# Performance work log

Measured on AMD Instinct MI355X. Metric: run time of the kernel, lower is better.

## Reference

```python
import jax, jax.numpy as jnp
import numpy as np

# ---- static config (matches init_kwargs and NSA hyperparams in source) ----
DIM = 512; HEADS = 8; DH = DIM // HEADS; DEPTH = 2
HH = 28; WW = 28; SEQ = HH * WW            # 784
WIN = 28 * 7                                # sliding window = 196
CBS = 28 * 14; CST = 28 * 7                 # compress block 392, stride 196
SBS = 28 * 14; NSEL = 1                     # selection block 392, top-1
NC = (SEQ - CBS) // CST + 1                 # 3 compressed blocks
NS = SEQ // SBS                             # 2 selection blocks
EPS = 1e-5
BATCH = 8


def _overlap_matrix():
    # fraction of each compressed block overlapping each selection block
    O = np.zeros((NC, NS), np.float32)
    for i in range(NC):
        a, b = i * CST, i * CST + CBS
        for j in range(NS):
            c, d = j * SBS, (j + 1) * SBS
            O[i, j] = max(0, min(b, d) - max(a, c)) / CBS
    return jnp.asarray(O)

OVERLAP = _overlap_matrix()  # [NC, NS]


def setup_inputs() -> dict:
    key = jax.random.key(0)
    ks = jax.random.split(key, 12)
    p = lambda i, shape, s=0.02: (jax.random.normal(ks[i], shape, jnp.float32) * s)
    return {
        "x": jax.random.normal(ks[0], (BATCH, DIM, HH, WW), jnp.float32),
        "pos_emb": jax.random.normal(ks[1], (SEQ,), jnp.float32),
        "attn_norm_g": jnp.ones((DEPTH, DIM), jnp.float32),
        "Wq": p(2, (DEPTH, DIM, HEADS * DH)),
        "Wk": p(3, (DEPTH, DIM, HEADS * DH)),
        "Wv": p(4, (DEPTH, DIM, HEADS * DH)),
        "Wo": p(5, (DEPTH, HEADS * DH, DIM)),
        "Wg": p(6, (DEPTH, DIM, HEADS * 3)),
        "ff_norm_g": jnp.ones((DEPTH, DIM), jnp.float32),
        "ff_norm_b": jnp.zeros((DEPTH, DIM), jnp.float32),
        "ff_w1": p(7, (DEPTH, 4 * DIM, DIM)),
        "ff_b1": jnp.zeros((DEPTH, 4 * DIM), jnp.float32),
        "ff_w2": p(8, (DEPTH, DIM, 4 * DIM)),
        "ff_b2": jnp.zeros((DEPTH, DIM), jnp.float32),
    }


def _sparse_attn(x, g, wq, wk, wv, wo, wg):
    # x: [b, n, d]  -- NSA: sliding window + compressed + top-k block selection
    b, n, d = x.shape
    xr = x * jax.lax.rsqrt(jnp.mean(x * x, -1, keepdims=True) + EPS) * g  # RMSNorm
    q = (xr @ wq).reshape(b, n, HEADS, DH)
    k = (xr @ wk).reshape(b, n, HEADS, DH)
    v = (xr @ wv).reshape(b, n, HEADS, DH)
    scale = DH ** -0.5

    # ---- compressed branch: mean-pool overlapping blocks ----
    ck = jnp.stack([k[:, i * CST:i * CST + CBS].mean(1) for i in range(NC)], 1)  # [b,NC,h,dh]
    cv = jnp.stack([v[:, i * CST:i * CST + CBS].mean(1) for i in range(NC)], 1)
    sc = jnp.einsum('bihd,bjhd->bhij', q, ck) * scale          # [b,h,n,NC]
    pc = jax.nn.softmax(sc, -1)
    out_c = jnp.einsum('bhij,bjhd->bihd', pc, cv)              # [b,n,h,dh]

    # ---- selection branch: importance -> top-k selection blocks -> fine attn ----
    imp = jnp.einsum('bhij,jk->bhik', pc, OVERLAP)             # [b,h,n,NS]
    _, sel = jax.lax.top_k(imp, NSEL)                          # [b,h,n,NSEL]
    selmask = jax.nn.one_hot(sel, NS, dtype=jnp.float32).sum(-2) > 0  # [b,h,n,NS]
    blk = jnp.arange(n) // SBS                                 # token -> selection block
    tokmask = selmask[..., blk]                                # [b,h,n,n]
    sf = jnp.einsum('bihd,bjhd->bhij', q, k) * scale           # full fine scores (shared)
    neg = jnp.finfo(sf.dtype).min
    ps = jax.nn.softmax(jnp.where(tokmask, sf, neg), -1)
    out_s = jnp.einsum('bhij,bjhd->bihd', ps, v)

    # ---- sliding window branch ----
    idx = jnp.arange(n)
    winmask = jnp.abs(idx[:, None] - idx[None, :]) < WIN       # [n,n]
    pw = jax.nn.softmax(jnp.where(winmask, sf, neg), -1)
    out_w = jnp.einsum('bhij,bjhd->bihd', pw, v)

    # ---- per-head learned gates over the 3 branches ----
    gates = jax.nn.sigmoid(xr @ wg).reshape(b, n, HEADS, 3)
    o = (gates[..., 0:1] * out_c + gates[..., 1:2] * out_s + gates[..., 2:3] * out_w)
    return o.reshape(b, n, HEADS * DH) @ wo


def _ff(x, g, bb, w1, b1, w2, b2):
    # x: [b,c,h,w]; LayerNorm over channel dim, then 1x1 conv -> GELU -> 1x1 conv
    mean = x.mean(1, keepdims=True)
    var = jnp.var(x, 1, keepdims=True)
    xn = (x - mean) / jnp.sqrt(var + EPS) * g[None, :, None, None] + bb[None, :, None, None]
    h1 = jax.nn.gelu(jnp.einsum('bchw,oc->bohw', xn, w1) + b1[None, :, None, None], approximate=False)
    return jnp.einsum('bchw,oc->bohw', h1, w2) + b2[None, :, None, None]


def reference(x, pos_emb, attn_norm_g, Wq, Wk, Wv, Wo, Wg,
              ff_norm_g, ff_norm_b, ff_w1, ff_b1, ff_w2, ff_b2):
    b, c, h, w = x.shape
    x = x + pos_emb[:h * w].reshape(1, 1, h, w)
    for l in range(DEPTH):
        s = x.reshape(b, c, h * w).transpose(0, 2, 1)          # b (h w) c
        s = _sparse_attn(s, attn_norm_g[l], Wq[l], Wk[l], Wv[l], Wo[l], Wg[l]) + s
        x = s.transpose(0, 2, 1).reshape(b, c, h, w)
        x = _ff(x, ff_norm_g[l], ff_norm_b[l], ff_w1[l], ff_b1[l], ff_w2[l], ff_b2[l]) + x
    return x
```

## Files before the change

kernel.cpp:

```cpp
#include <hip/hip_runtime.h>
#include <hip/hip_bf16.h>
#include <math.h>

#define B_      8
#define DIMC    512
#define SEQ_    784
#define HEADS_  8
#define DH_     64
#define NTOK    (B_*SEQ_)
#define QLD     1560
#define WIN_    196
#define CBS_    392
#define CST_    196
#define NC_     3
#define EPSF    1e-5f
#define FF_     2048
#define TQ_     28
#define MT_     98

typedef __hip_bfloat16 bf16_t;
typedef __attribute__((ext_vector_type(8))) short bf16x8;
typedef __attribute__((ext_vector_type(4))) float floatx4;
typedef __attribute__((ext_vector_type(4))) unsigned int uintx4;
typedef __attribute__((ext_vector_type(2))) unsigned int uintx2;

__device__ __forceinline__ float wsum(float x){
#pragma unroll
  for (int o = 32; o; o >>= 1) x += __shfl_xor(x, o, 64);
  return x;
}
__device__ __forceinline__ float geluf(float x){
  return 0.5f * x * (1.0f + erff(x * 0.70710678118654752f));
}
__device__ __forceinline__ float sigmoidf_(float x){
  return 1.0f / (1.0f + __expf(-x));
}

__global__ __launch_bounds__(256) void k_init(const float* __restrict__ xin,
                                              const float* __restrict__ pos,
                                              float* __restrict__ X){
  int idx = blockIdx.x * 256 + threadIdx.x;
  int c = idx & 511;
  int t = idx >> 9;
  int p = t % SEQ_;
  int b = t / SEQ_;
  float v = xin[((long)(b * DIMC + c)) * SEQ_ + p];
  X[idx] = v + pos[p];
}

__global__ __launch_bounds__(256) void k_final(const float* __restrict__ X,
                                               float* __restrict__ out){
  int idx = blockIdx.x * 256 + threadIdx.x;
  int p = idx % SEQ_;
  int t = idx / SEQ_;
  int c = t & 511;
  int b = t >> 9;
  out[idx] = X[((long)(b * SEQ_ + p)) * DIMC + c];
}

__global__ __launch_bounds__(256) void k_wconv1(const float* __restrict__ Wq,
                                                const float* __restrict__ Wk,
                                                const float* __restrict__ Wv,
                                                const float* __restrict__ Wg,
                                                bf16_t* __restrict__ Wb){
  int idx = blockIdx.x * 256 + threadIdx.x;
  int k = idx & 511;
  int t = idx >> 9;
  int n = t % QLD;
  int l = t / QLD;
  float v;
  if (n < 1536){
    int which = n >> 9;
    int nn = n & 511;
    const float* W = (which == 0) ? Wq : ((which == 1) ? Wk : Wv);
    v = W[((long)(l * 512 + k)) * 512 + nn];
  } else {
    v = Wg[((long)(l * 512 + k)) * 24 + (n - 1536)];
  }
  Wb[idx] = __float2bfloat16(v);
}

__global__ __launch_bounds__(256) void k_wconv2(const float* __restrict__ Wo,
                                                bf16_t* __restrict__ Wb){
  int idx = blockIdx.x * 256 + threadIdx.x;
  int k = idx & 511;
  int t = idx >> 9;
  int n = t & 511;
  int l = t >> 9;
  Wb[idx] = __float2bfloat16(Wo[((long)(l * 512 + k)) * 512 + n]);
}

__global__ __launch_bounds__(256) void k_cast(const float* __restrict__ src,
                                              bf16_t* __restrict__ dst){
  int idx = blockIdx.x * 256 + threadIdx.x;
  dst[idx] = __float2bfloat16(src[idx]);
}

__global__ __launch_bounds__(256) void k_zero(uintx4* __restrict__ p){
  p[blockIdx.x * 256 + threadIdx.x] = (uintx4){0u, 0u, 0u, 0u};
}

__global__ __launch_bounds__(256) void k_rms(const float* __restrict__ X,
                                             const float* __restrict__ g,
                                             bf16_t* __restrict__ XR){
  int tok = blockIdx.x;
  int tid = threadIdx.x;
  const float* xr = X + (long)tok * DIMC;
  float v0 = xr[tid], v1 = xr[tid + 256];
  float ss = v0 * v0 + v1 * v1;
  ss = wsum(ss);
  __shared__ float red[4];
  if ((tid & 63) == 0) red[tid >> 6] = ss;
  __syncthreads();
  float tot = red[0] + red[1] + red[2] + red[3];
  float r = rsqrtf(tot * (1.0f / DIMC) + EPSF);
  XR[(long)tok * DIMC + tid]       = __float2bfloat16(v0 * r * g[tid]);
  XR[(long)tok * DIMC + tid + 256] = __float2bfloat16(v1 * r * g[tid + 256]);
}

__global__ __launch_bounds__(256) void k_ln(const float* __restrict__ X,
                                            const float* __restrict__ g,
                                            const float* __restrict__ bb,
                                            bf16_t* __restrict__ XN){
  int tok = blockIdx.x;
  int tid = threadIdx.x;
  const float* xr = X + (long)tok * DIMC;
  float v0 = xr[tid], v1 = xr[tid + 256];
  float s = v0 + v1;
  float q = v0 * v0 + v1 * v1;
  s = wsum(s); q = wsum(q);
  __shared__ float r1[4], r2[4];
  if ((tid & 63) == 0){ r1[tid >> 6] = s; r2[tid >> 6] = q; }
  __syncthreads();
  float ts = r1[0] + r1[1] + r1[2] + r1[3];
  float tq = r2[0] + r2[1] + r2[2] + r2[3];
  float mean = ts * (1.0f / DIMC);
  float var  = tq * (1.0f / DIMC) - mean * mean;
  float rinv = rsqrtf(var + EPSF);
  XN[(long)tok * DIMC + tid]       = __float2bfloat16((v0 - mean) * rinv * g[tid]       + bb[tid]);
  XN[(long)tok * DIMC + tid + 256] = __float2bfloat16((v1 - mean) * rinv * g[tid + 256] + bb[tid + 256]);
}

template<int OUTBF, int ACT>
__global__ __launch_bounds__(256) void k_mgemm(const bf16_t* __restrict__ A,
                                               const bf16_t* __restrict__ Bm,
                                               float* Cf,
                                               bf16_t* Cb,
                                               const float* __restrict__ bias,
                                               const float* res,
                                               int M, int N, int K, int ldc, int ccol,
                                               bf16_t* VTo){
  int id = blockIdx.x;
  int xcd = id & 7;
  int j = id >> 3;
  int nt = j / 13;
  int mt = xcd * 13 + (j - nt * 13);
  if (mt >= MT_) return;
  int bm = mt * 64, bn = nt * 64;

  __shared__ bf16_t As[2][64][40];
  __shared__ bf16_t Bs[2][64][40];
  int tid = threadIdx.x;
  int w = tid >> 6, lane = tid & 63;
  int wm = (w & 1) * 32, wn = (w >> 1) * 32;
  int quad = lane >> 4, l16 = lane & 15;

  int lrow = tid >> 2, lkc = (tid & 3) * 8;
  bool bok = (bn + lrow) < N;
  const bf16_t* ap = A + (long)(bm + lrow) * K + lkc;
  const bf16_t* bp = Bm + (long)(bok ? bn + lrow : 0) * K + lkc;

  floatx4 acc[2][2];
#pragma unroll
  for (int i = 0; i < 2; i++)
#pragma unroll
    for (int jj = 0; jj < 2; jj++) acc[i][jj] = (floatx4)(0.0f);

  uintx4 areg = *(const uintx4*)ap;
  uintx4 breg = *(const uintx4*)bp;
  if (!bok) breg = (uintx4){0u,0u,0u,0u};

  int nch = K >> 5;
  for (int ch = 0; ch < nch; ch++){
    int buf = ch & 1;
    *(uintx4*)&As[buf][lrow][lkc] = areg;
    *(uintx4*)&Bs[buf][lrow][lkc] = breg;
    if (ch + 1 < nch){
      areg = *(const uintx4*)(ap + (ch + 1) * 32);
      breg = *(const uintx4*)(bp + (ch + 1) * 32);
      if (!bok) breg = (uintx4){0u,0u,0u,0u};
    }
    __syncthreads();
    bf16x8 a0 = *(bf16x8*)&As[buf][wm + l16][quad * 8];
    bf16x8 a1 = *(bf16x8*)&As[buf][wm + 16 + l16][quad * 8];
    bf16x8 b0 = *(bf16x8*)&Bs[buf][wn + l16][quad * 8];
    bf16x8 b1 = *(bf16x8*)&Bs[buf][wn + 16 + l16][quad * 8];
    acc[0][0] = __builtin_amdgcn_mfma_f32_16x16x32_bf16(a0, b0, acc[0][0], 0, 0, 0);
    acc[0][1] = __builtin_amdgcn_mfma_f32_16x16x32_bf16(a0, b1, acc[0][1], 0, 0, 0);
    acc[1][0] = __builtin_amdgcn_mfma_f32_16x16x32_bf16(a1, b0, acc[1][0], 0, 0, 0);
    acc[1][1] = __builtin_amdgcn_mfma_f32_16x16x32_bf16(a1, b1, acc[1][1], 0, 0, 0);
  }
#pragma unroll
  for (int tm = 0; tm < 2; tm++){
#pragma unroll
    for (int tn = 0; tn < 2; tn++){
      int ncol = bn + wn + tn * 16 + l16;
      if (ncol >= N) continue;
#pragma unroll
      for (int reg = 0; reg < 4; reg++){
        long mrow = bm + wm + tm * 16 + quad * 4 + reg;
        float v = acc[tm][tn][reg];
        if (bias) v += bias[ncol];
        if (ACT == 1) v = geluf(v);
        long off = mrow * (long)ldc + ccol + ncol;
        if (res) v += res[off];
        if (OUTBF){
          Cb[off] = __float2bfloat16(v);
          if (VTo && ncol >= 1024 && ncol < 1536){
            int bb2 = (int)mrow / SEQ_;
            int tok = (int)mrow - bb2 * SEQ_;
            VTo[((long)(bb2 * 512 + (ncol - 1024))) * 800 + tok] = __float2bfloat16(v);
          }
        }
        else       Cf[off] = v;
      }
    }
  }
}

__global__ __launch_bounds__(512) void k_cpool(const bf16_t* __restrict__ qkvg,
                                               float* __restrict__ ck,
                                               float* __restrict__ cv){
  int bj = blockIdx.x;
  int j = bj % NC_;
  int b = bj / NC_;
  int tid = threadIdx.x;
  int seg = tid & 127;
  int rg  = tid >> 7;
  __shared__ float part[4][1024];
  const bf16_t* base = qkvg + ((long)b * SEQ_ + (long)j * CST_) * QLD + 512;
  float acc[8] = {0.f,0.f,0.f,0.f,0.f,0.f,0.f,0.f};
  for (int r = rg; r < CBS_; r += 4){
    uintx4 v = *(const uintx4*)(base + (long)r * QLD + seg * 8);
    bf16_t tmp[8]; *(uintx4*)tmp = v;
#pragma unroll
    for (int q = 0; q < 8; q++) acc[q] += __bfloat162float(tmp[q]);
  }
#pragma unroll
  for (int q = 0; q < 8; q++) part[rg][seg * 8 + q] = acc[q];
  __syncthreads();
  for (int c = tid; c < 1024; c += 512){
    float s = (part[0][c] + part[1][c]) + (part[2][c] + part[3][c]);
    s *= (1.0f / CBS_);
    if (c < 512) ck[bj * DIMC + c] = s;
    else         cv[bj * DIMC + (c - 512)] = s;
  }
}

__global__ __launch_bounds__(256) void k_attn(const bf16_t* __restrict__ qkvg,
                                              const float* __restrict__ ck,
                                              const float* __restrict__ cv,
                                              const bf16_t* __restrict__ vtg,
                                              bf16_t* __restrict__ oattn){
  int tid = threadIdx.x;
  int w = tid >> 6, lane = tid & 63;
  int quad = lane >> 4, l16 = lane & 15;
  int id = blockIdx.x;
  int xcd = id & 7;
  int j = id >> 3;
  int bh = xcd * 8 + (j / 28);
  int i0 = (j % 28) * TQ_;
  int h = bh & 7, b = bh >> 3;
  const float scale = 0.125f;

  __shared__ __align__(16) char smem[77040];
  bf16_t (*Qs)[72]    = (bf16_t(*)[72])(smem);
  bf16_t (*Ks0)[72]   = (bf16_t(*)[72])(smem + 4608);
  bf16_t (*Ks1)[72]   = (bf16_t(*)[72])(smem + 13824);
  bf16_t (*sbuf)[808] = (bf16_t(*)[808])(smem + 23040);
  float  (*outc_s)[64]= (float(*)[64])(smem + 68288);
  int*   sel_s = (int*)(smem + 75456);
  float* cw_s  = (float*)(smem + 75568);
  float* cs_s  = (float*)(smem + 75680);
  float* g1_s  = (float*)(smem + 75792);
  float* g2_s  = (float*)(smem + 75904);
  float (*red_s)[4][16] = (float(*)[4][16])(smem + 76016);

  const long rowBase = (long)b * SEQ_ * QLD + h * 64;

  if (tid < 224){
    int q = tid >> 3, seg = tid & 7;
    uintx4 qv = *(const uintx4*)(qkvg + rowBase + (long)(i0 + q) * QLD + seg * 8);
    *(uintx4*)&Qs[q][seg * 8] = qv;
  } else {
    int u = tid - 224;
    int r = 28 + (u >> 3), seg = u & 7;
    *(uintx4*)&Qs[r][seg * 8] = (uintx4){0u, 0u, 0u, 0u};
  }
  __syncthreads();

  int r0i = tid >> 3, s0i = tid & 7;
  int r1i = 32 + r0i;
  uintx4 kreg0 = *(const uintx4*)(qkvg + rowBase + (long)r0i * QLD + 512 + s0i * 8);
  uintx4 kreg1 = *(const uintx4*)(qkvg + rowBase + (long)r1i * QLD + 512 + s0i * 8);

  {
    const float* CKp = ck + (long)b * NC_ * DIMC + h * 64 + lane;
    const float* CVp = cv + (long)b * NC_ * DIMC + h * 64 + lane;
    float k0 = CKp[0], k1 = CKp[512], k2 = CKp[1024];
    float v0 = CVp[0], v1 = CVp[512], v2 = CVp[1024];
#pragma unroll
    for (int qp = 0; qp < 7; qp++){
      int qg = w * 7 + qp;
      float qd = __bfloat162float(Qs[qg][lane]);
      float s0 = wsum(qd * k0) * scale;
      float s1 = wsum(qd * k1) * scale;
      float s2 = wsum(qd * k2) * scale;
      float m3 = fmaxf(s0, fmaxf(s1, s2));
      float e0 = __expf(s0 - m3), e1 = __expf(s1 - m3), e2 = __expf(s2 - m3);
      float inv = 1.0f / (e0 + e1 + e2);
      const bf16_t* grow = qkvg + (long)(b * SEQ_ + i0 + qg) * QLD + 1536 + h * 3;
      float g0 = sigmoidf_(__bfloat162float(grow[0]));
      float g1v = sigmoidf_(__bfloat162float(grow[1]));
      float g2v = sigmoidf_(__bfloat162float(grow[2]));
      outc_s[qg][lane] = g0 * (e0 * v0 + e1 * v1 + e2 * v2) * inv;
      int selv = (s2 > s0) ? 1 : 0;
      if (lane == 0){ sel_s[qg] = selv; g1_s[qg] = g1v; g2_s[qg] = g2v; }
    }
  }

  bf16x8 a00 = *(bf16x8*)&Qs[l16][quad * 8];
  bf16x8 a01 = *(bf16x8*)&Qs[l16][32 + quad * 8];
  bf16x8 a10 = *(bf16x8*)&Qs[16 + l16][quad * 8];
  bf16x8 a11 = *(bf16x8*)&Qs[16 + l16][32 + quad * 8];

  __syncthreads();

  int sel0i = sel_s[l16];
  int sel1i = (l16 < 12) ? sel_s[16 + l16] : 0;
  bool sv0 = (sel0i != 0), sv1 = (sel1i != 0);
  int iq0 = i0 + l16, iq1 = i0 + 16 + l16;
  float sw0 = 0.f, ss0 = 0.f, sw1 = 0.f, ss1 = 0.f;

  for (int ch = 0; ch < 13; ch++){
    bf16_t (*Kb)[72] = (ch & 1) ? Ks1 : Ks0;
    *(uintx4*)&Kb[r0i][s0i * 8] = kreg0;
    *(uintx4*)&Kb[r1i][s0i * 8] = kreg1;
    if (ch + 1 < 13){
      int c0n = (ch + 1) * 64;
      int t0 = c0n + r0i; if (t0 > 783) t0 = 783;
      int t1 = c0n + r1i; if (t1 > 783) t1 = 783;
      kreg0 = *(const uintx4*)(qkvg + rowBase + (long)t0 * QLD + 512 + s0i * 8);
      kreg1 = *(const uintx4*)(qkvg + rowBase + (long)t1 * QLD + 512 + s0i * 8);
    }
    __syncthreads();
    bf16x8 k0 = *(bf16x8*)&Kb[w * 16 + l16][quad * 8];
    bf16x8 k1 = *(bf16x8*)&Kb[w * 16 + l16][32 + quad * 8];
    floatx4 d0 = (floatx4)(0.0f), d1 = (floatx4)(0.0f);
    d0 = __builtin_amdgcn_mfma_f32_16x16x32_bf16(k0, a00, d0, 0, 0, 0);
    d0 = __builtin_amdgcn_mfma_f32_16x16x32_bf16(k1, a01, d0, 0, 0, 0);
    d1 = __builtin_amdgcn_mfma_f32_16x16x32_bf16(k0, a10, d1, 0, 0, 0);
    d1 = __builtin_amdgcn_mfma_f32_16x16x32_bf16(k1, a11, d1, 0, 0, 0);
    int kb = ch * 64 + w * 16 + quad * 4;
    union { bf16_t hh[4]; uintx2 v; } p0, p1;
#pragma unroll
    for (int r = 0; r < 4; r++){
      int key = kb + r;
      float ex0 = __expf(d0[r] * scale);
      float ex1 = __expf(d1[r] * scale);
      bool valid = key < 784;
      if (valid && key >= iq0 - 195 && key <= iq0 + 195) sw0 += ex0;
      if (valid && ((key >= 392) == sv0))                ss0 += ex0;
      if (valid && key >= iq1 - 195 && key <= iq1 + 195) sw1 += ex1;
      if (valid && ((key >= 392) == sv1))                ss1 += ex1;
      p0.hh[r] = __float2bfloat16(ex0);
      p1.hh[r] = __float2bfloat16(ex1);
    }
    if (kb < 784){
      *(uintx2*)&sbuf[l16][kb] = p0.v;
      if (l16 < 12) *(uintx2*)&sbuf[16 + l16][kb] = p1.v;
    }
  }

  sw0 += __shfl_xor(sw0, 16, 64); sw0 += __shfl_xor(sw0, 32, 64);
  ss0 += __shfl_xor(ss0, 16, 64); ss0 += __shfl_xor(ss0, 32, 64);
  sw1 += __shfl_xor(sw1, 16, 64); sw1 += __shfl_xor(sw1, 32, 64);
  ss1 += __shfl_xor(ss1, 16, 64); ss1 += __shfl_xor(ss1, 32, 64);
  if (quad == 0){
    red_s[w][0][l16] = sw0; red_s[w][1][l16] = ss0;
    red_s[w][2][l16] = sw1; red_s[w][3][l16] = ss1;
  }
  __syncthreads();
  if (tid < 28){
    int q = tid, t = q >> 4, l = q & 15;
    float sw = 0.f, ss = 0.f;
#pragma unroll
    for (int wv = 0; wv < 4; wv++){ sw += red_s[wv][2 * t][l]; ss += red_s[wv][2 * t + 1][l]; }
    cw_s[q] = g2_s[q] / sw;
    cs_s[q] = g1_s[q] / ss;
  }
  __syncthreads();

  const bf16_t* vrow = vtg + ((long)(b * 512 + h * 64 + w * 16 + l16)) * 800 + quad * 8;
  bf16x8 bv = *(const bf16x8*)vrow;

  for (int t = tid; t < 2800; t += 256){
    int q = t / 100;
    int c0 = (t - q * 100) * 8;
    uintx4 ov;
    if (c0 >= 784){
      ov = (uintx4){0u, 0u, 0u, 0u};
    } else {
      union { bf16_t hh[8]; uintx4 v; } in, out;
      in.v = *(uintx4*)&sbuf[q][c0];
      int iq = i0 + q;
      float cwv = cw_s[q], csv = cs_s[q];
      float cse = ((c0 >= 392) == (sel_s[q] != 0)) ? csv : 0.0f;
#pragma unroll
      for (int jj = 0; jj < 8; jj++){
        int c = c0 + jj;
        float coef = cse;
        if (c >= iq - 195 && c <= iq + 195) coef += cwv;
        out.hh[jj] = __float2bfloat16(__bfloat162float(in.hh[jj]) * coef);
      }
      ov = out.v;
    }
    *(uintx4*)&sbuf[q][c0] = ov;
  }
  __syncthreads();

  floatx4 o0 = (floatx4)(0.0f), o1 = (floatx4)(0.0f);
#pragma unroll 5
  for (int st = 0; st < 25; st++){
    bf16x8 bcur = bv;
    if (st + 1 < 25) bv = *(const bf16x8*)(vrow + (st + 1) * 32);
    int kc = st * 32 + quad * 8;
    bf16x8 av0 = *(bf16x8*)&sbuf[l16][kc];
    bf16x8 av1 = *(bf16x8*)&sbuf[16 + l16][kc];
    o0 = __builtin_amdgcn_mfma_f32_16x16x32_bf16(av0, bcur, o0, 0, 0, 0);
    o1 = __builtin_amdgcn_mfma_f32_16x16x32_bf16(av1, bcur, o1, 0, 0, 0);
  }

  int d = w * 16 + l16;
#pragma unroll
  for (int reg = 0; reg < 4; reg++){
    int q = quad * 4 + reg;
    float o = o0[reg] + outc_s[q][d];
    oattn[((long)(b * SEQ_ + i0 + q)) * DIMC + h * 64 + d] = __float2bfloat16(o);
    int q2 = q + 16;
    if (q2 < 28){
      float o2 = o1[reg] + outc_s[q2][d];
      oattn[((long)(b * SEQ_ + i0 + q2)) * DIMC + h * 64 + d] = __float2bfloat16(o2);
    }
  }
}

extern "C" void kernel_launch(void* const* d_in, const int* in_sizes, int n_in,
                              void* d_out, int out_size, void* d_ws, size_t ws_size,
                              hipStream_t stream){
  const float* xin  = (const float*)d_in[0];
  const float* pos  = (const float*)d_in[1];
  const float* angm = (const float*)d_in[2];
  const float* Wq   = (const float*)d_in[3];
  const float* Wk   = (const float*)d_in[4];
  const float* Wv   = (const float*)d_in[5];
  const float* Wo   = (const float*)d_in[6];
  const float* Wg   = (const float*)d_in[7];
  const float* fng  = (const float*)d_in[8];
  const float* fnb  = (const float*)d_in[9];
  const float* fw1  = (const float*)d_in[10];
  const float* fb1  = (const float*)d_in[11];
  const float* fw2  = (const float*)d_in[12];
  const float* fb2  = (const float*)d_in[13];

  char* cw = (char*)d_ws;
  float* X = (float*)cw;             cw += (long)NTOK * 512 * 4;
  bf16_t* XRb = (bf16_t*)cw;         cw += (long)NTOK * 512 * 2;
  bf16_t* OAb = (bf16_t*)cw;         cw += (long)NTOK * 512 * 2;
  bf16_t* SH  = (bf16_t*)cw;         cw += (long)NTOK * FF_ * 2;
  float* CK = (float*)cw;            cw += (long)B_ * NC_ * DIMC * 4;
  float* CV = (float*)cw;            cw += (long)B_ * NC_ * DIMC * 4;
  bf16_t* Wqkvgb = (bf16_t*)cw;      cw += (long)2 * QLD * 512 * 2;
  bf16_t* WOb    = (bf16_t*)cw;      cw += (long)2 * 512 * 512 * 2;
  bf16_t* FW1b   = (bf16_t*)cw;      cw += (long)2 * FF_ * 512 * 2;
  bf16_t* FW2b   = (bf16_t*)cw;      cw += (long)2 * 512 * FF_ * 2;
  bf16_t* VTb    = (bf16_t*)cw;      cw += (long)B_ * 512 * 800 * 2;
  bf16_t* BUFb = SH;
  bf16_t* H1b  = SH;

  k_wconv1<<<(2 * QLD * 512) / 256, 256, 0, stream>>>(Wq, Wk, Wv, Wg, Wqkvgb);
  k_wconv2<<<(2 * 512 * 512) / 256, 256, 0, stream>>>(Wo, WOb);
  k_cast<<<(2 * FF_ * 512) / 256, 256, 0, stream>>>(fw1, FW1b);
  k_cast<<<(2 * 512 * FF_) / 256, 256, 0, stream>>>(fw2, FW2b);

  k_zero<<<1600, 256, 0, stream>>>((uintx4*)VTb);

  k_init<<<12544, 256, 0, stream>>>(xin, pos, X);

  for (int l = 0; l < 2; l++){
    k_rms<<<NTOK, 256, 0, stream>>>(X, angm + (long)l * DIMC, XRb);

    k_mgemm<1, 0><<<25 * 104, 256, 0, stream>>>(
        XRb, Wqkvgb + (long)l * QLD * 512, nullptr, BUFb, nullptr, nullptr,
        NTOK, QLD, 512, QLD, 0, VTb);

    k_cpool<<<B_ * NC_, 512, 0, stream>>>(BUFb, CK, CV);

    k_attn<<<8 * 8 * 28, 256, 0, stream>>>(BUFb, CK, CV, VTb, OAb);

    k_mgemm<0, 0><<<8 * 104, 256, 0, stream>>>(
        OAb, WOb + (long)l * 512 * 512, X, nullptr, nullptr, X,
        NTOK, 512, 512, 512, 0, nullptr);

    k_ln<<<NTOK, 256, 0, stream>>>(X, fng + (long)l * DIMC, fnb + (long)l * DIMC, XRb);

    k_mgemm<1, 1><<<32 * 104, 256, 0, stream>>>(
        XRb, FW1b + (long)l * FF_ * 512, nullptr, H1b, fb1 + (long)l * FF_, nullptr,
        NTOK, FF_, 512, FF_, 0, nullptr);
    k_mgemm<0, 0><<<8 * 104, 256, 0, stream>>>(
        H1b, FW2b + (long)l * 512 * FF_, X, nullptr, fb2 + (long)l * DIMC, X,
        NTOK, 512, FF_, 512, 0, nullptr);
  }

  k_final<<<12544, 256, 0, stream>>>(X, (float*)d_out);
}
```

Baseline: 657.7 us.

## Enlarge GEMM tiles to 128x128 and stage operands with direct global-to-LDS loads

The shared bf16 MFMA GEMM moves from 64x64 to 128x128 output tiles, so each wave computes a 4x4 grid of 16x16 fragments instead of 2x2. This raises operand reuse per LDS load. Operand staging now uses global_load_lds to copy straight from global memory into double-buffered LDS, skipping the register round trip. The XCD-aware block remapping is generalised to arbitrary grid sizes and launch grids are recomputed. In exchange there are far fewer workgroups (e.g. 196 for the N=512 GEMMs), which may underfill the GPU's compute units, and there are more accumulator registers per thread.

```diff
diff --git a/kernel.cpp b/kernel.cpp
--- a/kernel.cpp
+++ b/kernel.cpp
@@ -16,7 +16,6 @@
 #define EPSF    1e-5f
 #define FF_     2048
 #define TQ_     28
-#define MT_     98
 
 typedef __hip_bfloat16 bf16_t;
 typedef __attribute__((ext_vector_type(8))) short bf16x8;
@@ -34,6 +33,11 @@
 }
 __device__ __forceinline__ float sigmoidf_(float x){
   return 1.0f / (1.0f + __expf(-x));
+}
+__device__ __forceinline__ void gload16(const bf16_t* g, bf16_t* l){
+  __builtin_amdgcn_global_load_lds(
+      (const __attribute__((address_space(1))) void*)g,
+      (__attribute__((address_space(3))) void*)l, 16, 0, 0);
 }
 
 __global__ __launch_bounds__(256) void k_init(const float* __restrict__ xin,
@@ -150,60 +154,73 @@
                                                const float* res,
                                                int M, int N, int K, int ldc, int ccol,
                                                bf16_t* VTo){
-  int id = blockIdx.x;
-  int xcd = id & 7;
-  int j = id >> 3;
-  int nt = j / 13;
-  int mt = xcd * 13 + (j - nt * 13);
-  if (mt >= MT_) return;
-  int bm = mt * 64, bn = nt * 64;
-
-  __shared__ bf16_t As[2][64][40];
-  __shared__ bf16_t Bs[2][64][40];
+  int nwg = gridDim.x;
+  int orig = blockIdx.x;
+  int qd = nwg >> 3, rm = nwg & 7;
+  int xcd = orig & 7, sidx = orig >> 3;
+  int wg = (xcd < rm ? xcd * (qd + 1) : rm * (qd + 1) + (xcd - rm) * qd) + sidx;
+  int mtiles = M >> 7;
+  int mt = wg % mtiles, nt = wg / mtiles;
+  int bm = mt * 128, bn = nt * 128;
+
+  __shared__ bf16_t As[2][128][32];
+  __shared__ bf16_t Bs[2][128][32];
+
   int tid = threadIdx.x;
   int w = tid >> 6, lane = tid & 63;
-  int wm = (w & 1) * 32, wn = (w >> 1) * 32;
   int quad = lane >> 4, l16 = lane & 15;
-
-  int lrow = tid >> 2, lkc = (tid & 3) * 8;
-  bool bok = (bn + lrow) < N;
-  const bf16_t* ap = A + (long)(bm + lrow) * K + lkc;
-  const bf16_t* bp = Bm + (long)(bok ? bn + lrow : 0) * K + lkc;
-
-  floatx4 acc[2][2];
-#pragma unroll
-  for (int i = 0; i < 2; i++)
-#pragma unroll
-    for (int jj = 0; jj < 2; jj++) acc[i][jj] = (floatx4)(0.0f);
-
-  uintx4 areg = *(const uintx4*)ap;
-  uintx4 breg = *(const uintx4*)bp;
-  if (!bok) breg = (uintx4){0u,0u,0u,0u};
+  int wm = (w & 1) * 64, wn = (w >> 1) * 64;
+
+  int srow = w * 32 + (lane >> 2);
+  int scol = (lane & 3) * 8;
+  const bf16_t* agp0 = A + (long)(bm + srow) * K + scol;
+  const bf16_t* agp1 = A + (long)(bm + srow + 16) * K + scol;
+  int br0 = bn + srow;      if (br0 >= N) br0 = N - 1;
+  int br1 = bn + srow + 16; if (br1 >= N) br1 = N - 1;
+  const bf16_t* bgp0 = Bm + (long)br0 * K + scol;
+  const bf16_t* bgp1 = Bm + (long)br1 * K + scol;
+
+  floatx4 acc[4][4];
+#pragma unroll
+  for (int i = 0; i < 4; i++)
+#pragma unroll
+    for (int jj = 0; jj < 4; jj++) acc[i][jj] = (floatx4)(0.0f);
 
   int nch = K >> 5;
+  gload16(agp0, &As[0][srow][scol]);
+  gload16(agp1, &As[0][srow + 16][scol]);
+  gload16(bgp0, &Bs[0][srow][scol]);
+  gload16(bgp1, &Bs[0][srow + 16][scol]);
+  __syncthreads();
+
+  int cur = 0;
   for (int ch = 0; ch < nch; ch++){
-    int buf = ch & 1;
-    *(uintx4*)&As[buf][lrow][lkc] = areg;
-    *(uintx4*)&Bs[buf][lrow][lkc] = breg;
     if (ch + 1 < nch){
-      areg = *(const uintx4*)(ap + (ch + 1) * 32);
-      breg = *(const uintx4*)(bp + (ch + 1) * 32);
-      if (!bok) breg = (uintx4){0u,0u,0u,0u};
-    }
+      int ko = (ch + 1) * 32;
+      gload16(agp0 + ko, &As[cur ^ 1][srow][scol]);
+      gload16(agp1 + ko, &As[cur ^ 1][srow + 16][scol]);
+      gload16(bgp0 + ko, &Bs[cur ^ 1][srow][scol]);
+      gload16(bgp1 + ko, &Bs[cur ^ 1][srow + 16][scol]);
+    }
+    bf16x8 af[4], bfr[4];
+#pragma unroll
+    for (int f = 0; f < 4; f++){
+      af[f]  = *(bf16x8*)&As[cur][wm + f * 16 + l16][quad * 8];
+      bfr[f] = *(bf16x8*)&Bs[cur][wn + f * 16 + l16][quad * 8];
+    }
+#pragma unroll
+    for (int i = 0; i < 4; i++)
+#pragma unroll
+      for (int jj = 0; jj < 4; jj++)
+        acc[i][jj] = __builtin_amdgcn_mfma_f32_16x16x32_bf16(af[i], bfr[jj], acc[i][jj], 0, 0, 0);
     __syncthreads();
-    bf16x8 a0 = *(bf16x8*)&As[buf][wm + l16][quad * 8];
-    bf16x8 a1 = *(bf16x8*)&As[buf][wm + 16 + l16][quad * 8];
-    bf16x8 b0 = *(bf16x8*)&Bs[buf][wn + l16][quad * 8];
-    bf16x8 b1 = *(bf16x8*)&Bs[buf][wn + 16 + l16][quad * 8];
-    acc[0][0] = __builtin_amdgcn_mfma_f32_16x16x32_bf16(a0, b0, acc[0][0], 0, 0, 0);
-    acc[0][1] = __builtin_amdgcn_mfma_f32_16x16x32_bf16(a0, b1, acc[0][1], 0, 0, 0);
-    acc[1][0] = __builtin_amdgcn_mfma_f32_16x16x32_bf16(a1, b0, acc[1][0], 0, 0, 0);
-    acc[1][1] = __builtin_amdgcn_mfma_f32_16x16x32_bf16(a1, b1, acc[1][1], 0, 0, 0);
-  }
-#pragma unroll
-  for (int tm = 0; tm < 2; tm++){
-#pragma unroll
-    for (int tn = 0; tn < 2; tn++){
+    cur ^= 1;
+  }
+
+#pragma unroll
+  for (int tm = 0; tm < 4; tm++){
+#pragma unroll
+    for (int tn = 0; tn < 4; tn++){
       int ncol = bn + wn + tn * 16 + l16;
       if (ncol >= N) continue;
 #pragma unroll
@@ -217,8 +234,8 @@
         if (OUTBF){
           Cb[off] = __float2bfloat16(v);
           if (VTo && ncol >= 1024 && ncol < 1536){
-            int bb2 = (int)mrow / SEQ_;
-            int tok = (int)mrow - bb2 * SEQ_;
+            int bb2 = (int)(mrow / SEQ_);
+            int tok = (int)(mrow - (long)bb2 * SEQ_);
             VTo[((long)(bb2 * 512 + (ncol - 1024))) * 800 + tok] = __float2bfloat16(v);
           }
         }
@@ -500,7 +517,7 @@
   for (int l = 0; l < 2; l++){
     k_rms<<<NTOK, 256, 0, stream>>>(X, angm + (long)l * DIMC, XRb);
 
-    k_mgemm<1, 0><<<25 * 104, 256, 0, stream>>>(
+    k_mgemm<1, 0><<<49 * 13, 256, 0, stream>>>(
         XRb, Wqkvgb + (long)l * QLD * 512, nullptr, BUFb, nullptr, nullptr,
         NTOK, QLD, 512, QLD, 0, VTb);
 
@@ -508,16 +525,16 @@
 
     k_attn<<<8 * 8 * 28, 256, 0, stream>>>(BUFb, CK, CV, VTb, OAb);
 
-    k_mgemm<0, 0><<<8 * 104, 256, 0, stream>>>(
+    k_mgemm<0, 0><<<49 * 4, 256, 0, stream>>>(
         OAb, WOb + (long)l * 512 * 512, X, nullptr, nullptr, X,
         NTOK, 512, 512, 512, 0, nullptr);
 
     k_ln<<<NTOK, 256, 0, stream>>>(X, fng + (long)l * DIMC, fnb + (long)l * DIMC, XRb);
 
-    k_mgemm<1, 1><<<32 * 104, 256, 0, stream>>>(
+    k_mgemm<1, 1><<<49 * 16, 256, 0, stream>>>(
         XRb, FW1b + (long)l * FF_ * 512, nullptr, H1b, fb1 + (long)l * FF_, nullptr,
         NTOK, FF_, 512, FF_, 0, nullptr);
-    k_mgemm<0, 0><<<8 * 104, 256, 0, stream>>>(
+    k_mgemm<0, 0><<<49 * 4, 256, 0, stream>>>(
         H1b, FW2b + (long)l * 512 * FF_, X, nullptr, fb2 + (long)l * DIMC, X,
         NTOK, 512, FF_, 512, 0, nullptr);
   }
```

Measured after the change: 783.7 us. 1.19x slower.
